# Kernel tuning notes

Hardware: AMD Instinct MI355X
Metric: run time of the kernel (lower is better)

Reference implementation:

```python
import jax, jax.numpy as jnp
import numpy as np

N_NODES = 100000
N_EDGES = 1600000
IN_C, HID_C, OUT_C = 128, 64, 40
BN_EPS = 1e-5


def setup_inputs() -> dict:
    key = jax.random.key(0)
    ks = jax.random.split(key, 12)
    def lin(k, fan_in, fan_out):
        bound = 1.0 / np.sqrt(fan_in)
        return jax.random.uniform(k, (fan_in, fan_out), jnp.float32, -bound, bound)
    x = jax.random.normal(ks[0], (N_NODES, IN_C), jnp.float32)
    edge_index = jax.random.randint(ks[1], (2, N_EDGES), 0, N_NODES, jnp.int64)
    return {
        "x": x,
        "edge_index": edge_index,
        "W1": lin(ks[2], IN_C, HID_C), "b1": jnp.zeros((HID_C,), jnp.float32),
        "g1": jnp.ones((HID_C,), jnp.float32), "be1": jnp.zeros((HID_C,), jnp.float32),
        "W2": lin(ks[3], HID_C, HID_C), "b2": jnp.zeros((HID_C,), jnp.float32),
        "g2": jnp.ones((HID_C,), jnp.float32), "be2": jnp.zeros((HID_C,), jnp.float32),
        "W3": lin(ks[4], HID_C, OUT_C), "b3": jnp.zeros((OUT_C,), jnp.float32),
    }


def _gcn_conv(h, W, b, src, dst, edge_norm, self_norm):
    # linear transform then symmetric-normalized aggregation (GCN with self loops)
    h = h @ W + b
    msg = h[src] * edge_norm[:, None]                      # [E, C] gather
    agg = jax.ops.segment_sum(msg, dst, num_segments=N_NODES)  # scatter-add
    return agg + h * self_norm[:, None]


def _bn_relu(h, gamma, beta):
    mu = jnp.mean(h, axis=0)
    var = jnp.mean(jnp.square(h - mu), axis=0)
    return jax.nn.relu((h - mu) * jax.lax.rsqrt(var + BN_EPS) * gamma + beta)


def reference(x, edge_index, W1, b1, g1, be1, W2, b2, g2, be2, W3, b3):
    src, dst = edge_index[0], edge_index[1]
    # degree with self loops (computed on dst, as in PyG GCNConv)
    deg = jax.ops.segment_sum(jnp.ones((N_EDGES,), x.dtype), dst,
                              num_segments=N_NODES) + 1.0
    dis = jax.lax.rsqrt(deg)
    edge_norm = dis[src] * dis[dst]   # [E]
    self_norm = 1.0 / deg             # [N]

    h = _gcn_conv(x, W1, b1, src, dst, edge_norm, self_norm)
    h = _bn_relu(h, g1, be1)
    h = _gcn_conv(h, W2, b2, src, dst, edge_norm, self_norm)
    h = _bn_relu(h, g2, be2)
    h = _gcn_conv(h, W3, b3, src, dst, edge_norm, self_norm)
    return h
```

## Files before the change

### kernel.cpp

```cpp
#include <hip/hip_runtime.h>

#define N_NODES 100000
#define N_EDGES 1600000
#define NBKT 391
#define EPB 4096
#define NBLK_E ((N_EDGES + EPB - 1) / EPB)

typedef unsigned short u16;
typedef unsigned int u32;
typedef u32 u32x4 __attribute__((ext_vector_type(4)));
struct alignas(8) bf4 { u16 a, b, c, d; };

__device__ __forceinline__ float blo(u32 u) { return __uint_as_float(u << 16); }
__device__ __forceinline__ float bhi(u32 u) { return __uint_as_float(u & 0xffff0000u); }
__device__ __forceinline__ u16 f2bf(float f) {
  u32 u = __float_as_uint(f);
  return (u16)((u + 0x7fffu + ((u >> 16) & 1u)) >> 16);
}
__device__ __forceinline__ u32 pack2(float a, float b) {
  return (u32)f2bf(a) | ((u32)f2bf(b) << 16);
}


__global__ __launch_bounds__(256) void bucket_count_k(const int* __restrict__ dst,
                                                      int* __restrict__ gCount) {
  __shared__ int h[NBKT];
  for (int i = threadIdx.x; i < NBKT; i += 256) h[i] = 0;
  __syncthreads();
  const int e0 = blockIdx.x * EPB;
  const int eN = min(EPB, N_EDGES - e0);
  for (int i = threadIdx.x; i < eN; i += 256) atomicAdd(&h[dst[e0 + i] >> 8], 1);
  __syncthreads();
  for (int i = threadIdx.x; i < NBKT; i += 256)
    if (h[i]) atomicAdd(&gCount[i], h[i]);
}

__global__ void bucket_scan_k(const int* __restrict__ gCount,
                              int* __restrict__ gBase,
                              int* __restrict__ gCursor,
                              int* __restrict__ offsets) {
  __shared__ int sm[512];
  const int t = threadIdx.x;
  const int c0 = (t < NBKT) ? gCount[t] : 0;
  const int c1 = (t + 256 < NBKT) ? gCount[t + 256] : 0;
  sm[t] = c0; sm[t + 256] = c1;
  __syncthreads();
  for (int off = 1; off < 512; off <<= 1) {
    const int v0 = (t >= off) ? sm[t - off] : 0;
    const int v1 = (t + 256 >= off) ? sm[t + 256 - off] : 0;
    __syncthreads();
    sm[t] += v0; sm[t + 256] += v1;
    __syncthreads();
  }
  if (t < NBKT)       { const int b = sm[t] - c0;       gBase[t] = b;       gCursor[t] = b; }
  if (t + 256 < NBKT) { const int b = sm[t + 256] - c1; gBase[t + 256] = b; gCursor[t + 256] = b; }
  if (t == 0) { gBase[NBKT] = N_EDGES; offsets[N_NODES] = N_EDGES; }
}

__global__ __launch_bounds__(256) void bucket_scatter_k(const int* __restrict__ src,
                                                        const int* __restrict__ dst,
                                                        int* __restrict__ gCursor,
                                                        uint2* __restrict__ ebuf) {
  __shared__ int cnt[NBKT];
  __shared__ int inc[512];
  __shared__ int gb[NBKT];
  __shared__ int cur[NBKT];
  __shared__ uint2 st[EPB];
  const int t = threadIdx.x;
  for (int i = t; i < NBKT; i += 256) cnt[i] = 0;
  __syncthreads();
  const int e0 = blockIdx.x * EPB;
  const int eN = min(EPB, N_EDGES - e0);
  for (int i = t; i < eN; i += 256) atomicAdd(&cnt[dst[e0 + i] >> 8], 1);
  __syncthreads();
  const int c0 = (t < NBKT) ? cnt[t] : 0;
  const int c1 = (t + 256 < NBKT) ? cnt[t + 256] : 0;
  inc[t] = c0; inc[t + 256] = c1;
  __syncthreads();
  for (int off = 1; off < 512; off <<= 1) {
    const int v0 = (t >= off) ? inc[t - off] : 0;
    const int v1 = (t + 256 >= off) ? inc[t + 256 - off] : 0;
    __syncthreads();
    inc[t] += v0; inc[t + 256] += v1;
    __syncthreads();
  }
  if (t < NBKT) {
    if (c0) gb[t] = atomicAdd(&gCursor[t], c0);
    cur[t] = inc[t] - c0;
  }
  if (t + 256 < NBKT) {
    if (c1) gb[t + 256] = atomicAdd(&gCursor[t + 256], c1);
    cur[t + 256] = inc[t + 256] - c1;
  }
  __syncthreads();
  for (int i = t; i < eN; i += 256) {
    const int d = dst[e0 + i];
    const int b = d >> 8;
    const int p = atomicAdd(&cur[b], 1);
    st[p] = make_uint2((unsigned)src[e0 + i], (unsigned)d);
  }
  __syncthreads();
  for (int i = t; i < eN; i += 256) {
    const uint2 e = st[i];
    const int b = (int)(e.y >> 8);
    const int excl = inc[b] - cnt[b];
    ebuf[gb[b] + (i - excl)] = e;
  }
}

__global__ __launch_bounds__(256) void csr_build_k(const uint2* __restrict__ ebuf,
                                                   const int* __restrict__ gBase,
                                                   int* __restrict__ offsets,
                                                   int* __restrict__ csr_src,
                                                   float* __restrict__ dis,
                                                   float* __restrict__ selfn) {
  __shared__ int cnt[256];
  __shared__ int inc[256];
  __shared__ int cur[256];
  const int t = threadIdx.x;
  const int b = blockIdx.x;
  const int ebeg = gBase[b], eend = gBase[b + 1];
  cnt[t] = 0;
  __syncthreads();
  for (int e = ebeg + t; e < eend; e += 256) atomicAdd(&cnt[ebuf[e].y & 255], 1);
  __syncthreads();
  const int c = cnt[t];
  inc[t] = c;
  __syncthreads();
  for (int off = 1; off < 256; off <<= 1) {
    const int v = (t >= off) ? inc[t - off] : 0;
    __syncthreads();
    inc[t] += v;
    __syncthreads();
  }
  const int node = (b << 8) + t;
  const int goff = ebeg + inc[t] - c;
  cur[t] = goff;
  if (node < N_NODES) {
    offsets[node] = goff;
    const float deg = (float)c + 1.0f;
    dis[node] = rsqrtf(deg);
    selfn[node] = 1.0f / deg;
  }
  __syncthreads();
  for (int e = ebeg + t; e < eend; e += 256) {
    const uint2 ed = ebuf[e];
    const int p = atomicAdd(&cur[ed.y & 255], 1);
    csr_src[p] = (int)ed.x;
  }
}

__global__ __launch_bounds__(256) void pack_k(const int* __restrict__ csr_src,
                                              const float* __restrict__ dis,
                                              int2* __restrict__ csr2) {
  const int i = blockIdx.x * 256 + threadIdx.x;
  if (i < N_EDGES) {
    const int v = csr_src[i] & 0xFFFFF;
    csr2[i] = make_int2(v, __float_as_int(dis[v]));
  }
}


template <int K, int C, int RPT, bool BN, bool BF16IN>
__global__ __launch_bounds__(256) void gemm_k(const void* __restrict__ Av,
                                              const float* __restrict__ W,
                                              const float* __restrict__ bias,
                                              const float* __restrict__ scale,
                                              const float* __restrict__ shift,
                                              u16* __restrict__ out) {
  constexpr int CQ = C / 4;
  constexpr int TR = 256 / CQ;
  constexpr int ROWS = TR * RPT;
  __shared__ __align__(16) float Wl[K * C];
  __shared__ __align__(16) float Al[ROWS * K];
  const int tid = threadIdx.x;
  for (int i = tid; i < K * C; i += 256) Wl[i] = W[i];
  const int row0 = blockIdx.x * ROWS;
  for (int i = tid; i < ROWS * K / 4; i += 256) {
    const int e0 = i * 4;
    const int r = e0 / K, k = e0 - (e0 / K) * K;
    const int gr = row0 + r;
    float v0 = 0.f, v1 = 0.f, v2 = 0.f, v3 = 0.f;
    if (gr < N_NODES) {
      if (BF16IN) {
        const uint2 u = *(const uint2*)((const u16*)Av + (size_t)gr * K + k);
        v0 = blo(u.x); v1 = bhi(u.x); v2 = blo(u.y); v3 = bhi(u.y);
      } else {
        const float4 a = *(const float4*)((const float*)Av + (size_t)gr * K + k);
        v0 = a.x; v1 = a.y; v2 = a.z; v3 = a.w;
      }
      if (BN) {
        const float4 sc = *(const float4*)(scale + k);
        const float4 sh = *(const float4*)(shift + k);
        v0 = fmaxf(fmaf(v0, sc.x, sh.x), 0.f);
        v1 = fmaxf(fmaf(v1, sc.y, sh.y), 0.f);
        v2 = fmaxf(fmaf(v2, sc.z, sh.z), 0.f);
        v3 = fmaxf(fmaf(v3, sc.w, sh.w), 0.f);
      }
    }
    *(float4*)(Al + r * K + k) = make_float4(v0, v1, v2, v3);
  }
  __syncthreads();
  const int cq = tid % CQ;
  const int rs = tid / CQ;
  if (rs >= TR) return;
  const float4* W4 = (const float4*)Wl;
  const float4* A4 = (const float4*)Al;
  float4 acc[RPT];
#pragma unroll
  for (int i = 0; i < RPT; ++i) acc[i] = make_float4(0.f, 0.f, 0.f, 0.f);
#pragma unroll 4
  for (int k4 = 0; k4 < K / 4; ++k4) {
    float4 w0 = W4[(4 * k4 + 0) * CQ + cq];
    float4 w1 = W4[(4 * k4 + 1) * CQ + cq];
    float4 w2 = W4[(4 * k4 + 2) * CQ + cq];
    float4 w3 = W4[(4 * k4 + 3) * CQ + cq];
#pragma unroll
    for (int i = 0; i < RPT; ++i) {
      float4 a = A4[(rs * RPT + i) * (K / 4) + k4];
      acc[i].x = fmaf(a.x, w0.x, acc[i].x); acc[i].y = fmaf(a.x, w0.y, acc[i].y);
      acc[i].z = fmaf(a.x, w0.z, acc[i].z); acc[i].w = fmaf(a.x, w0.w, acc[i].w);
      acc[i].x = fmaf(a.y, w1.x, acc[i].x); acc[i].y = fmaf(a.y, w1.y, acc[i].y);
      acc[i].z = fmaf(a.y, w1.z, acc[i].z); acc[i].w = fmaf(a.y, w1.w, acc[i].w);
      acc[i].x = fmaf(a.z, w2.x, acc[i].x); acc[i].y = fmaf(a.z, w2.y, acc[i].y);
      acc[i].z = fmaf(a.z, w2.z, acc[i].z); acc[i].w = fmaf(a.z, w2.w, acc[i].w);
      acc[i].x = fmaf(a.w, w3.x, acc[i].x); acc[i].y = fmaf(a.w, w3.y, acc[i].y);
      acc[i].z = fmaf(a.w, w3.z, acc[i].z); acc[i].w = fmaf(a.w, w3.w, acc[i].w);
    }
  }
  float4 b4 = ((const float4*)bias)[cq];
#pragma unroll
  for (int i = 0; i < RPT; ++i) {
    int gr = row0 + rs * RPT + i;
    if (gr < N_NODES) {
      bf4 o;
      o.a = f2bf(acc[i].x + b4.x); o.b = f2bf(acc[i].y + b4.y);
      o.c = f2bf(acc[i].z + b4.z); o.d = f2bf(acc[i].w + b4.w);
      *(bf4*)(out + (size_t)gr * C + cq * 4) = o;
    }
  }
}


template <bool STATS>
__global__ __launch_bounds__(256) void agg64_v4_k(const u16* __restrict__ tb,
                                                  const int2* __restrict__ csr2,
                                                  const int* __restrict__ offs,
                                                  const float* __restrict__ dis,
                                                  const float* __restrict__ selfn,
                                                  u16* __restrict__ out,
                                                  float* __restrict__ part) {
  __shared__ float s_sum[64];
  __shared__ float s_sq[64];
  if (STATS) {
    if (threadIdx.x < 64) { s_sum[threadIdx.x] = 0.f; s_sq[threadIdx.x] = 0.f; }
    __syncthreads();
  }
  const int lane = threadIdx.x & 63;
  const int nb = (blockIdx.x * 4 + (threadIdx.x >> 6)) * 4;
  const int g = lane >> 3;
  const int c4 = lane & 7;
  const int i = g >> 1;
  const int p = g & 1;
  const int node = nb + i;
  int beg = 0, end = 0;
  if (node < N_NODES) { beg = offs[node]; end = offs[node + 1]; }
  int iters = (end - beg + 1) >> 1;
  iters = max(iters, __shfl_xor(iters, 8));
  iters = max(iters, __shfl_xor(iters, 16));
  iters = max(iters, __shfl_xor(iters, 32));
  float acc[8];
#pragma unroll
  for (int k = 0; k < 8; ++k) acc[k] = 0.f;
  const u16* __restrict__ tc = tb + (c4 << 3);
  int e = beg + p;
#pragma unroll 4
  for (int it = 0; it < iters; ++it) {
    int2 ev = make_int2(0, 0);
    if (e < end) ev = csr2[e];
    e += 2;
    const int s = ev.x & 0xFFFFF;
    const float w = __int_as_float(ev.y);
    const u32x4 q = __builtin_nontemporal_load((const u32x4*)(tc + (size_t)s * 64));
    acc[0] = fmaf(blo(q.x), w, acc[0]);
    acc[1] = fmaf(bhi(q.x), w, acc[1]);
    acc[2] = fmaf(blo(q.y), w, acc[2]);
    acc[3] = fmaf(bhi(q.y), w, acc[3]);
    acc[4] = fmaf(blo(q.z), w, acc[4]);
    acc[5] = fmaf(bhi(q.z), w, acc[5]);
    acc[6] = fmaf(blo(q.w), w, acc[6]);
    acc[7] = fmaf(bhi(q.w), w, acc[7]);
  }
#pragma unroll
  for (int k = 0; k < 8; ++k) acc[k] += __shfl_xor(acc[k], 8);
  float v[8];
  const bool writer = (p == 0) && (node < N_NODES);
  if (writer) {
    const float dn = dis[node], sn = selfn[node];
    const uint4 q = *(const uint4*)(tb + (size_t)node * 64 + (c4 << 3));
    const float sv[8] = {blo(q.x), bhi(q.x), blo(q.y), bhi(q.y),
                         blo(q.z), bhi(q.z), blo(q.w), bhi(q.w)};
#pragma unroll
    for (int k = 0; k < 8; ++k) v[k] = fmaf(dn, acc[k], sv[k] * sn);
    uint4 o;
    o.x = pack2(v[0], v[1]); o.y = pack2(v[2], v[3]);
    o.z = pack2(v[4], v[5]); o.w = pack2(v[6], v[7]);
    *(uint4*)(out + (size_t)node * 64 + (c4 << 3)) = o;
  }
  if (STATS) {
    if (writer) {
#pragma unroll
      for (int k = 0; k < 8; ++k) {
        atomicAdd(&s_sum[(c4 << 3) + k], v[k]);
        atomicAdd(&s_sq[(c4 << 3) + k], v[k] * v[k]);
      }
    }
    __syncthreads();
    if (threadIdx.x < 128) {
      const int c = threadIdx.x & 63;
      const float val = (threadIdx.x < 64) ? s_sum[c] : s_sq[c];
      atomicAdd(&part[(blockIdx.x & 63) * 128 + (threadIdx.x < 64 ? c : 64 + c)], val);
    }
  }
}

__global__ __launch_bounds__(256) void agg40_v4_k(const u16* __restrict__ tb,
                                                  const int2* __restrict__ csr2,
                                                  const int* __restrict__ offs,
                                                  const float* __restrict__ dis,
                                                  const float* __restrict__ selfn,
                                                  float* __restrict__ out) {
  const int lane = threadIdx.x & 63;
  const int nb = (blockIdx.x * 4 + (threadIdx.x >> 6)) * 4;
  const bool ok = lane < 60;
  const int g = ok ? (lane / 5) : 0;
  const int c4 = ok ? (lane - g * 5) : 0;
  const int i = g / 3;
  const int p = g - i * 3;
  const int node = nb + i;
  int beg = 0, end = 0;
  if (ok && node < N_NODES) { beg = offs[node]; end = offs[node + 1]; }
  int iters = (end - beg + 2) / 3;
  iters = max(iters, __shfl_xor(iters, 1));
  iters = max(iters, __shfl_xor(iters, 2));
  iters = max(iters, __shfl_xor(iters, 4));
  iters = max(iters, __shfl_xor(iters, 8));
  iters = max(iters, __shfl_xor(iters, 16));
  iters = max(iters, __shfl_xor(iters, 32));
  float acc[8];
#pragma unroll
  for (int k = 0; k < 8; ++k) acc[k] = 0.f;
  const u16* __restrict__ tc = tb + (c4 << 3);
  int e = beg + p;
#pragma unroll 4
  for (int it = 0; it < iters; ++it) {
    int2 ev = make_int2(0, 0);
    if (e < end) ev = csr2[e];
    e += 3;
    const int s = ev.x & 0xFFFFF;
    const float w = __int_as_float(ev.y);
    const u32x4 q = __builtin_nontemporal_load((const u32x4*)(tc + (size_t)s * 40));
    acc[0] = fmaf(blo(q.x), w, acc[0]);
    acc[1] = fmaf(bhi(q.x), w, acc[1]);
    acc[2] = fmaf(blo(q.y), w, acc[2]);
    acc[3] = fmaf(bhi(q.y), w, acc[3]);
    acc[4] = fmaf(blo(q.z), w, acc[4]);
    acc[5] = fmaf(bhi(q.z), w, acc[5]);
    acc[6] = fmaf(blo(q.w), w, acc[6]);
    acc[7] = fmaf(bhi(q.w), w, acc[7]);
  }
  const int base = 15 * i + c4;
  float tot[8];
#pragma unroll
  for (int k = 0; k < 8; ++k) {
    tot[k] = __shfl(acc[k], base) + __shfl(acc[k], base + 5) + __shfl(acc[k], base + 10);
  }
  if (ok && p == 0 && node < N_NODES) {
    const float dn = dis[node], sn = selfn[node];
    const uint4 q = *(const uint4*)(tb + (size_t)node * 40 + (c4 << 3));
    const float sv[8] = {blo(q.x), bhi(q.x), blo(q.y), bhi(q.y),
                         blo(q.z), bhi(q.z), blo(q.w), bhi(q.w)};
    float v[8];
#pragma unroll
    for (int k = 0; k < 8; ++k) v[k] = fmaf(dn, tot[k], sv[k] * sn);
    float4* op = (float4*)(out + (size_t)node * 40 + (c4 << 3));
    op[0] = make_float4(v[0], v[1], v[2], v[3]);
    op[1] = make_float4(v[4], v[5], v[6], v[7]);
  }
}

__global__ void bnfinal_k(const float* __restrict__ part, const float* __restrict__ g,
                          const float* __restrict__ be, float* __restrict__ scale,
                          float* __restrict__ shift) {
  const int c = threadIdx.x;
  float s = 0.f, q = 0.f;
  for (int b = 0; b < 64; ++b) { s += part[b * 128 + c]; q += part[b * 128 + 64 + c]; }
  const float inv = 1.0f / (float)N_NODES;
  const float mu = s * inv;
  const float var = q * inv - mu * mu;
  const float sc = g[c] * rsqrtf(var + 1e-5f);
  scale[c] = sc;
  shift[c] = fmaf(-mu, sc, be[c]);
}


extern "C" void kernel_launch(void* const* d_in, const int* in_sizes, int n_in,
                              void* d_out, int out_size, void* d_ws, size_t ws_size,
                              hipStream_t stream) {
  const float* x   = (const float*)d_in[0];
  const int*   ei  = (const int*)d_in[1];
  const float* W1  = (const float*)d_in[2];
  const float* b1  = (const float*)d_in[3];
  const float* g1  = (const float*)d_in[4];
  const float* be1 = (const float*)d_in[5];
  const float* W2  = (const float*)d_in[6];
  const float* b2  = (const float*)d_in[7];
  const float* g2  = (const float*)d_in[8];
  const float* be2 = (const float*)d_in[9];
  const float* W3  = (const float*)d_in[10];
  const float* b3  = (const float*)d_in[11];
  float* out = (float*)d_out;
  const int* src = ei;
  const int* dst = ei + N_EDGES;

  char* ws = (char*)d_ws;
  size_t o = 0;
  auto alloc = [&](size_t bytes) -> char* {
    char* p = ws + o;
    o += (bytes + 255) & ~(size_t)255;
    return p;
  };
  int*   gCount  = (int*)alloc((size_t)NBKT * 4);
  int*   gBase   = (int*)alloc(((size_t)NBKT + 1) * 4);
  int*   gCursor = (int*)alloc((size_t)NBKT * 4);
  int*   offsets = (int*)alloc(((size_t)N_NODES + 1) * 4);
  int*   csr_src = (int*)alloc((size_t)N_EDGES * 4);
  float* dis     = (float*)alloc((size_t)N_NODES * 4);
  float* selfn   = (float*)alloc((size_t)N_NODES * 4);
  float* part1   = (float*)alloc(64 * 128 * 4);
  float* part2   = (float*)alloc(64 * 128 * 4);
  float* scale1  = (float*)alloc(64 * 4);
  float* shift1  = (float*)alloc(64 * 4);
  float* scale2  = (float*)alloc(64 * 4);
  float* shift2  = (float*)alloc(64 * 4);
  char*  treg    = alloc((size_t)N_NODES * 64 * 4);
  u16*   hbuf    = (u16*)alloc((size_t)N_NODES * 64 * 2);
  u16*  tbuf = (u16*)treg;
  uint2* ebuf = (uint2*)treg;
  int2* csr2 = (int2*)(treg + (size_t)N_NODES * 64 * 2);

  hipMemsetAsync(gCount, 0, (size_t)NBKT * 4, stream);
  hipMemsetAsync(part1, 0, 2 * 64 * 128 * 4, stream);

  bucket_count_k<<<NBLK_E, 256, 0, stream>>>(dst, gCount);
  bucket_scan_k<<<1, 256, 0, stream>>>(gCount, gBase, gCursor, offsets);
  bucket_scatter_k<<<NBLK_E, 256, 0, stream>>>(src, dst, gCursor, ebuf);
  csr_build_k<<<NBKT, 256, 0, stream>>>(ebuf, gBase, offsets, csr_src, dis, selfn);
  pack_k<<<(N_EDGES + 255) / 256, 256, 0, stream>>>(csr_src, dis, csr2);

  const int nagg = (N_NODES + 15) / 16;

  gemm_k<128, 64, 2, false, false><<<(N_NODES + 31) / 32, 256, 0, stream>>>(
      x, W1, b1, nullptr, nullptr, tbuf);
  agg64_v4_k<true><<<nagg, 256, 0, stream>>>(
      tbuf, csr2, offsets, dis, selfn, hbuf, part1);
  bnfinal_k<<<1, 64, 0, stream>>>(part1, g1, be1, scale1, shift1);

  gemm_k<64, 64, 4, true, true><<<(N_NODES + 63) / 64, 256, 0, stream>>>(
      hbuf, W2, b2, scale1, shift1, tbuf);
  agg64_v4_k<true><<<nagg, 256, 0, stream>>>(
      tbuf, csr2, offsets, dis, selfn, hbuf, part2);
  bnfinal_k<<<1, 64, 0, stream>>>(part2, g2, be2, scale2, shift2);

  gemm_k<64, 40, 4, true, true><<<(N_NODES + 99) / 100, 256, 0, stream>>>(
      hbuf, W3, b3, scale2, shift2, tbuf);
  agg40_v4_k<<<nagg, 256, 0, stream>>>(
      tbuf, csr2, offsets, dis, selfn, out);
}
```

Measured before the change: 539.7 us.

## Use bf16 MFMA for node GEMMs, drop nontemporal gathers, parallelize BN finalize

Replaces the scalar-FMA fp32 GEMM with a bf16 MFMA 16x16x32 kernel that converts the input and weight tiles to bf16 in padded shared memory. Each wave computes 16 rows across all output column tiles. The change also switches the aggregation gathers from nontemporal loads to normal cached loads, so reused rows can hit in cache. It also spreads the BN partial reduction over 256 threads. Rounding the GEMM inputs to bf16 reduces precision, and the GEMM epilogue now writes scalar, non-vectorized stores.

```diff
diff --git a/kernel.cpp b/kernel.cpp
--- a/kernel.cpp
+++ b/kernel.cpp
@@ -8,7 +8,8 @@
 
 typedef unsigned short u16;
 typedef unsigned int u32;
-typedef u32 u32x4 __attribute__((ext_vector_type(4)));
+typedef short bf16x8 __attribute__((ext_vector_type(8)));
+typedef float f32x4 __attribute__((ext_vector_type(4)));
 struct alignas(8) bf4 { u16 a, b, c, d; };
 
 __device__ __forceinline__ float blo(u32 u) { return __uint_as_float(u << 16); }
@@ -161,22 +162,25 @@
 }
 
 
-template <int K, int C, int RPT, bool BN, bool BF16IN>
-__global__ __launch_bounds__(256) void gemm_k(const void* __restrict__ Av,
-                                              const float* __restrict__ W,
-                                              const float* __restrict__ bias,
-                                              const float* __restrict__ scale,
-                                              const float* __restrict__ shift,
-                                              u16* __restrict__ out) {
-  constexpr int CQ = C / 4;
-  constexpr int TR = 256 / CQ;
-  constexpr int ROWS = TR * RPT;
-  __shared__ __align__(16) float Wl[K * C];
-  __shared__ __align__(16) float Al[ROWS * K];
+template <int K, int C, bool BN, bool BF16IN>
+__global__ __launch_bounds__(256) void gemm_mfma_k(const void* __restrict__ Av,
+                                                   const float* __restrict__ W,
+                                                   const float* __restrict__ bias,
+                                                   const float* __restrict__ scale,
+                                                   const float* __restrict__ shift,
+                                                   u16* __restrict__ out) {
+  constexpr int CPAD = (C + 15) & ~15;
+  constexpr int CT = CPAD / 16;
+  constexpr int KS = K + 8;
+  __shared__ u16 Al[64 * KS];
+  __shared__ u16 Wt[CPAD * KS];
   const int tid = threadIdx.x;
-  for (int i = tid; i < K * C; i += 256) Wl[i] = W[i];
-  const int row0 = blockIdx.x * ROWS;
-  for (int i = tid; i < ROWS * K / 4; i += 256) {
+  const int row0 = blockIdx.x * 64;
+  for (int i = tid; i < K * C; i += 256) {
+    const int k = i / C, c = i - k * C;
+    Wt[c * KS + k] = f2bf(W[i]);
+  }
+  for (int i = tid; i < 64 * K / 4; i += 256) {
     const int e0 = i * 4;
     const int r = e0 / K, k = e0 - (e0 / K) * K;
     const int gr = row0 + r;
@@ -198,58 +202,51 @@
         v3 = fmaxf(fmaf(v3, sc.w, sh.w), 0.f);
       }
     }
-    *(float4*)(Al + r * K + k) = make_float4(v0, v1, v2, v3);
-  }
-  __syncthreads();
-  const int cq = tid % CQ;
-  const int rs = tid / CQ;
-  if (rs >= TR) return;
-  const float4* W4 = (const float4*)Wl;
-  const float4* A4 = (const float4*)Al;
-  float4 acc[RPT];
-#pragma unroll
-  for (int i = 0; i < RPT; ++i) acc[i] = make_float4(0.f, 0.f, 0.f, 0.f);
-#pragma unroll 4
-  for (int k4 = 0; k4 < K / 4; ++k4) {
-    float4 w0 = W4[(4 * k4 + 0) * CQ + cq];
-    float4 w1 = W4[(4 * k4 + 1) * CQ + cq];
-    float4 w2 = W4[(4 * k4 + 2) * CQ + cq];
-    float4 w3 = W4[(4 * k4 + 3) * CQ + cq];
-#pragma unroll
-    for (int i = 0; i < RPT; ++i) {
-      float4 a = A4[(rs * RPT + i) * (K / 4) + k4];
-      acc[i].x = fmaf(a.x, w0.x, acc[i].x); acc[i].y = fmaf(a.x, w0.y, acc[i].y);
-      acc[i].z = fmaf(a.x, w0.z, acc[i].z); acc[i].w = fmaf(a.x, w0.w, acc[i].w);
-      acc[i].x = fmaf(a.y, w1.x, acc[i].x); acc[i].y = fmaf(a.y, w1.y, acc[i].y);
-      acc[i].z = fmaf(a.y, w1.z, acc[i].z); acc[i].w = fmaf(a.y, w1.w, acc[i].w);
-      acc[i].x = fmaf(a.z, w2.x, acc[i].x); acc[i].y = fmaf(a.z, w2.y, acc[i].y);
-      acc[i].z = fmaf(a.z, w2.z, acc[i].z); acc[i].w = fmaf(a.z, w2.w, acc[i].w);
-      acc[i].x = fmaf(a.w, w3.x, acc[i].x); acc[i].y = fmaf(a.w, w3.y, acc[i].y);
-      acc[i].z = fmaf(a.w, w3.z, acc[i].z); acc[i].w = fmaf(a.w, w3.w, acc[i].w);
+    ushort4 pk;
+    pk.x = f2bf(v0); pk.y = f2bf(v1); pk.z = f2bf(v2); pk.w = f2bf(v3);
+    *(ushort4*)(Al + r * KS + k) = pk;
+  }
+  __syncthreads();
+  const int wv = tid >> 6;
+  const int lane = tid & 63;
+  const int mr = lane & 15;
+  const int kq = lane >> 4;
+  f32x4 acc[CT];
+#pragma unroll
+  for (int t = 0; t < CT; ++t) acc[t] = (f32x4){0.f, 0.f, 0.f, 0.f};
+  const u16* ab = Al + (wv * 16 + mr) * KS + kq * 8;
+#pragma unroll
+  for (int ks = 0; ks < K; ks += 32) {
+    const bf16x8 af = *(const bf16x8*)(ab + ks);
+#pragma unroll
+    for (int t = 0; t < CT; ++t) {
+      const bf16x8 bf = *(const bf16x8*)(Wt + (t * 16 + mr) * KS + kq * 8 + ks);
+      acc[t] = __builtin_amdgcn_mfma_f32_16x16x32_bf16(af, bf, acc[t], 0, 0, 0);
     }
   }
-  float4 b4 = ((const float4*)bias)[cq];
-#pragma unroll
-  for (int i = 0; i < RPT; ++i) {
-    int gr = row0 + rs * RPT + i;
-    if (gr < N_NODES) {
-      bf4 o;
-      o.a = f2bf(acc[i].x + b4.x); o.b = f2bf(acc[i].y + b4.y);
-      o.c = f2bf(acc[i].z + b4.z); o.d = f2bf(acc[i].w + b4.w);
-      *(bf4*)(out + (size_t)gr * C + cq * 4) = o;
+#pragma unroll
+  for (int t = 0; t < CT; ++t) {
+    const int col = t * 16 + mr;
+    if (col < C) {
+      const float bb = bias[col];
+#pragma unroll
+      for (int r = 0; r < 4; ++r) {
+        const int gr = row0 + wv * 16 + kq * 4 + r;
+        if (gr < N_NODES) out[(size_t)gr * C + col] = f2bf(acc[t][r] + bb);
+      }
     }
   }
 }
 
 
 template <bool STATS>
-__global__ __launch_bounds__(256) void agg64_v4_k(const u16* __restrict__ tb,
-                                                  const int2* __restrict__ csr2,
-                                                  const int* __restrict__ offs,
-                                                  const float* __restrict__ dis,
-                                                  const float* __restrict__ selfn,
-                                                  u16* __restrict__ out,
-                                                  float* __restrict__ part) {
+__global__ __launch_bounds__(256) void agg64_k(const u16* __restrict__ tb,
+                                               const int2* __restrict__ csr2,
+                                               const int* __restrict__ offs,
+                                               const float* __restrict__ dis,
+                                               const float* __restrict__ selfn,
+                                               u16* __restrict__ out,
+                                               float* __restrict__ part) {
   __shared__ float s_sum[64];
   __shared__ float s_sq[64];
   if (STATS) {
@@ -281,7 +278,7 @@
     e += 2;
     const int s = ev.x & 0xFFFFF;
     const float w = __int_as_float(ev.y);
-    const u32x4 q = __builtin_nontemporal_load((const u32x4*)(tc + (size_t)s * 64));
+    const uint4 q = *(const uint4*)(tc + (size_t)s * 64);
     acc[0] = fmaf(blo(q.x), w, acc[0]);
     acc[1] = fmaf(bhi(q.x), w, acc[1]);
     acc[2] = fmaf(blo(q.y), w, acc[2]);
@@ -324,12 +321,12 @@
   }
 }
 
-__global__ __launch_bounds__(256) void agg40_v4_k(const u16* __restrict__ tb,
-                                                  const int2* __restrict__ csr2,
-                                                  const int* __restrict__ offs,
-                                                  const float* __restrict__ dis,
-                                                  const float* __restrict__ selfn,
-                                                  float* __restrict__ out) {
+__global__ __launch_bounds__(256) void agg40_k(const u16* __restrict__ tb,
+                                               const int2* __restrict__ csr2,
+                                               const int* __restrict__ offs,
+                                               const float* __restrict__ dis,
+                                               const float* __restrict__ selfn,
+                                               float* __restrict__ out) {
   const int lane = threadIdx.x & 63;
   const int nb = (blockIdx.x * 4 + (threadIdx.x >> 6)) * 4;
   const bool ok = lane < 60;
@@ -359,7 +356,7 @@
     e += 3;
     const int s = ev.x & 0xFFFFF;
     const float w = __int_as_float(ev.y);
-    const u32x4 q = __builtin_nontemporal_load((const u32x4*)(tc + (size_t)s * 40));
+    const uint4 q = *(const uint4*)(tc + (size_t)s * 40);
     acc[0] = fmaf(blo(q.x), w, acc[0]);
     acc[1] = fmaf(bhi(q.x), w, acc[1]);
     acc[2] = fmaf(blo(q.y), w, acc[2]);
@@ -392,15 +389,26 @@
 __global__ void bnfinal_k(const float* __restrict__ part, const float* __restrict__ g,
                           const float* __restrict__ be, float* __restrict__ scale,
                           float* __restrict__ shift) {
-  const int c = threadIdx.x;
+  __shared__ float ss[256], qq[256];
+  const int c = threadIdx.x & 63;
+  const int qa = threadIdx.x >> 6;
   float s = 0.f, q = 0.f;
-  for (int b = 0; b < 64; ++b) { s += part[b * 128 + c]; q += part[b * 128 + 64 + c]; }
-  const float inv = 1.0f / (float)N_NODES;
-  const float mu = s * inv;
-  const float var = q * inv - mu * mu;
-  const float sc = g[c] * rsqrtf(var + 1e-5f);
-  scale[c] = sc;
-  shift[c] = fmaf(-mu, sc, be[c]);
+  for (int b = qa * 16; b < qa * 16 + 16; ++b) {
+    s += part[b * 128 + c];
+    q += part[b * 128 + 64 + c];
+  }
+  ss[threadIdx.x] = s; qq[threadIdx.x] = q;
+  __syncthreads();
+  if (threadIdx.x < 64) {
+    s = ss[c] + ss[c + 64] + ss[c + 128] + ss[c + 192];
+    q = qq[c] + qq[c + 64] + qq[c + 128] + qq[c + 192];
+    const float inv = 1.0f / (float)N_NODES;
+    const float mu = s * inv;
+    const float var = q * inv - mu * mu;
+    const float sc = g[c] * rsqrtf(var + 1e-5f);
+    scale[c] = sc;
+    shift[c] = fmaf(-mu, sc, be[c]);
+  }
 }
 
 
@@ -459,21 +467,22 @@
   pack_k<<<(N_EDGES + 255) / 256, 256, 0, stream>>>(csr_src, dis, csr2);
 
   const int nagg = (N_NODES + 15) / 16;
-
-  gemm_k<128, 64, 2, false, false><<<(N_NODES + 31) / 32, 256, 0, stream>>>(
+  const int ngemm = (N_NODES + 63) / 64;
+
+  gemm_mfma_k<128, 64, false, false><<<ngemm, 256, 0, stream>>>(
       x, W1, b1, nullptr, nullptr, tbuf);
-  agg64_v4_k<true><<<nagg, 256, 0, stream>>>(
+  agg64_k<true><<<nagg, 256, 0, stream>>>(
       tbuf, csr2, offsets, dis, selfn, hbuf, part1);
-  bnfinal_k<<<1, 64, 0, stream>>>(part1, g1, be1, scale1, shift1);
-
-  gemm_k<64, 64, 4, true, true><<<(N_NODES + 63) / 64, 256, 0, stream>>>(
+  bnfinal_k<<<1, 256, 0, stream>>>(part1, g1, be1, scale1, shift1);
+
+  gemm_mfma_k<64, 64, true, true><<<ngemm, 256, 0, stream>>>(
       hbuf, W2, b2, scale1, shift1, tbuf);
-  agg64_v4_k<true><<<nagg, 256, 0, stream>>>(
+  agg64_k<true><<<nagg, 256, 0, stream>>>(
       tbuf, csr2, offsets, dis, selfn, hbuf, part2);
-  bnfinal_k<<<1, 64, 0, stream>>>(part2, g2, be2, scale2, shift2);
-
-  gemm_k<64, 40, 4, true, true><<<(N_NODES + 99) / 100, 256, 0, stream>>>(
+  bnfinal_k<<<1, 256, 0, stream>>>(part2, g2, be2, scale2, shift2);
+
+  gemm_mfma_k<64, 40, true, true><<<ngemm, 256, 0, stream>>>(
       hbuf, W3, b3, scale2, shift2, tbuf);
-  agg40_v4_k<<<nagg, 256, 0, stream>>>(
+  agg40_k<<<nagg, 256, 0, stream>>>(
       tbuf, csr2, offsets, dis, selfn, out);
 }
```

Result: faster. 454.4 us (-15.8%).
